# Kernel optimization log

Measured on AMD Instinct MI355X. Metric: run time of the kernel, lower is better.

## Reference

```python
import jax, jax.numpy as jnp
import numpy as np

L, D, H, B, N = 4, 1024, 16, 4, 1024
DK = D // H
BN_EPS = 1e-5


def conv1x1(x, W, b):
    # x: (B, C_in, N), W: (C_out, C_in), b: (C_out,)
    return jnp.einsum('oc,bcn->bon', W, x) + b[:, None]


def setup_inputs() -> dict:
    key = jax.random.key(0)
    ks = jax.random.split(key, 17)
    s = 0.02
    inp = {
        'motion_feats': jax.random.normal(ks[0], (B, D, N), dtype=jnp.float32),
        'Wq': jax.random.normal(ks[1], (L, D, D), dtype=jnp.float32) * s,
        'bq': jax.random.normal(ks[2], (L, D), dtype=jnp.float32) * s,
        'Wk': jax.random.normal(ks[3], (L, D, D), dtype=jnp.float32) * s,
        'bk': jax.random.normal(ks[4], (L, D), dtype=jnp.float32) * s,
        'Wv': jax.random.normal(ks[5], (L, D, D), dtype=jnp.float32) * s,
        'bv': jax.random.normal(ks[6], (L, D), dtype=jnp.float32) * s,
        'Wm': jax.random.normal(ks[7], (L, D, D), dtype=jnp.float32) * s,
        'bm': jax.random.normal(ks[8], (L, D), dtype=jnp.float32) * s,
        'Wp1': jax.random.normal(ks[9], (L, 2 * D, 2 * D), dtype=jnp.float32) * s,
        'bp1': jax.random.normal(ks[10], (L, 2 * D), dtype=jnp.float32) * s,
        'bn_gamma': 1.0 + 0.1 * jax.random.normal(ks[11], (L, 2 * D), dtype=jnp.float32),
        'bn_beta': 0.1 * jax.random.normal(ks[12], (L, 2 * D), dtype=jnp.float32),
        'bn_mean': 0.1 * jax.random.normal(ks[13], (L, 2 * D), dtype=jnp.float32),
        'bn_var': 0.5 + jax.random.uniform(ks[14], (L, 2 * D), dtype=jnp.float32),
        'Wp2': jax.random.normal(ks[15], (L, D, 2 * D), dtype=jnp.float32) * s,
        'bp2': jnp.zeros((L, D), dtype=jnp.float32),  # init.constant_(bias, 0)
    }
    return inp


def _mha_layer(x, Wq, bq, Wk, bk, Wv, bv, Wm, bm, Wp1, bp1, g, bta, mu, var, Wp2, bp2):
    # x: (B, D, N)
    q = conv1x1(x, Wq, bq).reshape(B, DK, H, N)
    k = conv1x1(x, Wk, bk).reshape(B, DK, H, N)
    v = conv1x1(x, Wv, bv).reshape(B, DK, H, N)
    scores = jnp.einsum('bdhn,bdhm->bhnm', q, k) / jnp.sqrt(jnp.float32(DK))
    w = jax.nn.softmax(scores, axis=-1)
    attn = jnp.einsum('bhnm,bdhm->bdhn', w, v).reshape(B, D, N)
    merged = conv1x1(attn, Wm, bm)
    h = jnp.concatenate([merged, x], axis=1)  # (B, 2D, N)
    h = conv1x1(h, Wp1, bp1)
    # BatchNorm1d in eval mode (running stats)
    h = g[:, None] * (h - mu[:, None]) * jax.lax.rsqrt(var[:, None] + BN_EPS) + bta[:, None]
    h = jax.nn.relu(h)
    return conv1x1(h, Wp2, bp2)


def reference(motion_feats, Wq, bq, Wk, bk, Wv, bv, Wm, bm, Wp1, bp1,
              bn_gamma, bn_beta, bn_mean, bn_var, Wp2, bp2):
    x = motion_feats
    for l in range(L):
        attn_out = _mha_layer(x, Wq[l], bq[l], Wk[l], bk[l], Wv[l], bv[l],
                              Wm[l], bm[l], Wp1[l], bp1[l],
                              bn_gamma[l], bn_beta[l], bn_mean[l], bn_var[l],
                              Wp2[l], bp2[l])
        x = x + attn_out
    return x
```

## Files before the change

### kernel.cpp

```cpp
#include <hip/hip_runtime.h>

typedef unsigned short u16;
typedef __attribute__((ext_vector_type(8))) short bf16x8;
typedef __attribute__((ext_vector_type(4))) float f32x4;

#define B_ 4
#define D_ 1024
#define N_ 1024
#define H_ 16
#define DK_ 64

__device__ inline float bf2f(u16 x) {
    union { unsigned u; float f; } c; c.u = ((unsigned)x) << 16; return c.f;
}
__device__ inline u16 f2bf(float f) {
    union { float f; unsigned u; } c; c.f = f;
    unsigned r = c.u + 0x7fff + ((c.u >> 16) & 1);
    return (u16)(r >> 16);
}

#if __has_builtin(__builtin_amdgcn_exp2f)
#define EXP2(x) __builtin_amdgcn_exp2f(x)
#else
#define EXP2(x) __expf((x) * 0.6931471805599453f)
#endif

__device__ inline bf16x8 load8(const void* p, size_t idx, int fl) {
    if (!fl) return *(const bf16x8*)((const u16*)p + idx);
    const float* fp = (const float*)p + idx;
    f32x4 a = *(const f32x4*)fp;
    f32x4 b = *(const f32x4*)(fp + 4);
    bf16x8 r;
    #pragma unroll
    for (int j = 0; j < 4; ++j) {
        ((u16*)&r)[j]     = f2bf(a[j]);
        ((u16*)&r)[4 + j] = f2bf(b[j]);
    }
    return r;
}

__global__ __launch_bounds__(256) void k_cvt(
    const float* __restrict__ src, u16* __restrict__ dst, int n8)
{
    int i = blockIdx.x * 256 + threadIdx.x;
    if (i < n8) {
        const f32x4* s = (const f32x4*)src;
        f32x4 a = s[2 * i], b = s[2 * i + 1];
        bf16x8 r;
        #pragma unroll
        for (int j = 0; j < 4; ++j) {
            ((u16*)&r)[j]     = f2bf(a[j]);
            ((u16*)&r)[4 + j] = f2bf(b[j]);
        }
        ((bf16x8*)dst)[i] = r;
    }
}

__device__ __forceinline__ void gload16(const u16* g, u16* l) {
    __builtin_amdgcn_global_load_lds(
        (const __attribute__((address_space(1))) void*)g,
        (__attribute__((address_space(3))) void*)l, 16, 0, 0);
}

template<int ROWS>
__device__ __forceinline__ void stage_rows(const u16* __restrict__ g, int ld,
                                           int k0, u16* L, int wave)
{
    #pragma unroll
    for (int i = 0; i < ROWS / 64; ++i)
        gload16(g + (size_t)(i * 64) * ld + k0, L + i * 2048 + wave * 512);
}

template<int MT, int NT>
__device__ inline void gemm_bf16(const u16* __restrict__ A, int lda,
                                 const u16* __restrict__ Bt, size_t eoff,
                                 int ldb, int K, int m0, int n0,
                                 u16* lds, f32x4 acc[MT/32][NT/32])
{
    constexpr int FM = MT / 32, FN = NT / 32;
    constexpr int TSZ = (MT + NT) * 32;
    const int tid  = threadIdx.x;
    const int wave = tid >> 6, lane = tid & 63;
    const int quad = lane >> 4, l15 = lane & 15;
    const int wm = (wave >> 1) * (MT / 2);
    const int wn = (wave & 1) * (NT / 2);

    const u16* ga = A + (size_t)(m0 + (tid >> 2)) * lda + ((tid & 3) << 3);
    const u16* gb = Bt + eoff + (size_t)(n0 + (tid >> 2)) * ldb + ((tid & 3) << 3);

    stage_rows<MT>(ga, lda, 0, lds, wave);
    stage_rows<NT>(gb, ldb, 0, lds + MT * 32, wave);
    __syncthreads();

    int buf = 0;
    for (int k0 = 0; k0 < K; k0 += 32) {
        const u16* La = lds + buf * TSZ;
        const u16* Lb = La + MT * 32;

        if (k0 + 32 < K) {
            u16* Na = lds + (buf ^ 1) * TSZ;
            stage_rows<MT>(ga, lda, k0 + 32, Na, wave);
            stage_rows<NT>(gb, ldb, k0 + 32, Na + MT * 32, wave);
        }

        bf16x8 af[FM], bv[FN];
        #pragma unroll
        for (int f = 0; f < FM; ++f)
            af[f] = *(const bf16x8*)&La[(wm + f * 16 + l15) * 32 + quad * 8];
        #pragma unroll
        for (int f = 0; f < FN; ++f)
            bv[f] = *(const bf16x8*)&Lb[(wn + f * 16 + l15) * 32 + quad * 8];
        #pragma unroll
        for (int fm = 0; fm < FM; ++fm)
            #pragma unroll
            for (int fn = 0; fn < FN; ++fn)
                acc[fm][fn] = __builtin_amdgcn_mfma_f32_16x16x32_bf16(
                    af[fm], bv[fn], acc[fm][fn], 0, 0, 0);

        __syncthreads();
        buf ^= 1;
    }
}

template<int MT, int NT>
__device__ inline void gemm_core(const u16* __restrict__ A, int lda,
                                 const void* __restrict__ Bt, size_t eoff,
                                 int ldb, int fl,
                                 int K, int m0, int n0,
                                 u16* lds, f32x4 acc[MT/32][NT/32])
{
    constexpr int FM = MT / 32, FN = NT / 32;
    constexpr int CA = MT * 4 / 256, CB = NT * 4 / 256;
    const int tid  = threadIdx.x;
    const int wave = tid >> 6, lane = tid & 63;
    const int quad = lane >> 4, l15 = lane & 15;
    const int wm = (wave >> 1) * (MT / 2);
    const int wn = (wave & 1) * (NT / 2);

    int arow[CA], acol[CA], brow[CB], bcol[CB];
    #pragma unroll
    for (int i = 0; i < CA; ++i) { int x = tid + i * 256; arow[i] = x >> 2; acol[i] = (x & 3) << 3; }
    #pragma unroll
    for (int i = 0; i < CB; ++i) { int x = tid + i * 256; brow[i] = x >> 2; bcol[i] = (x & 3) << 3; }

    bf16x8 pa[CA], pb[CB];
    #pragma unroll
    for (int i = 0; i < CA; ++i)
        pa[i] = *(const bf16x8*)(A + (size_t)(m0 + arow[i]) * lda + acol[i]);
    #pragma unroll
    for (int i = 0; i < CB; ++i)
        pb[i] = load8(Bt, eoff + (size_t)(n0 + brow[i]) * ldb + bcol[i], fl);

    int buf = 0;
    for (int k0 = 0; k0 < K; k0 += 32) {
        u16* La = lds + buf * ((MT + NT) * 40);
        u16* Lb = La + MT * 40;
        #pragma unroll
        for (int i = 0; i < CA; ++i) *(bf16x8*)&La[arow[i] * 40 + acol[i]] = pa[i];
        #pragma unroll
        for (int i = 0; i < CB; ++i) *(bf16x8*)&Lb[brow[i] * 40 + bcol[i]] = pb[i];
        __syncthreads();

        if (k0 + 32 < K) {
            #pragma unroll
            for (int i = 0; i < CA; ++i)
                pa[i] = *(const bf16x8*)(A + (size_t)(m0 + arow[i]) * lda + k0 + 32 + acol[i]);
            #pragma unroll
            for (int i = 0; i < CB; ++i)
                pb[i] = load8(Bt, eoff + (size_t)(n0 + brow[i]) * ldb + k0 + 32 + bcol[i], fl);
        }

        bf16x8 af[FM], bv[FN];
        #pragma unroll
        for (int f = 0; f < FM; ++f)
            af[f] = *(bf16x8*)&La[(wm + f * 16 + l15) * 40 + quad * 8];
        #pragma unroll
        for (int f = 0; f < FN; ++f)
            bv[f] = *(bf16x8*)&Lb[(wn + f * 16 + l15) * 40 + quad * 8];
        #pragma unroll
        for (int fm = 0; fm < FM; ++fm)
            #pragma unroll
            for (int fn = 0; fn < FN; ++fn)
                acc[fm][fn] = __builtin_amdgcn_mfma_f32_16x16x32_bf16(
                    af[fm], bv[fn], acc[fm][fn], 0, 0, 0);
        buf ^= 1;
    }
}

#define EPI_SETUP \
    const int tid = threadIdx.x; \
    const int wave = tid >> 6, lane = tid & 63; \
    const int quad = lane >> 4, l15 = lane & 15;

__global__ __launch_bounds__(256) void k_qkv(
    const u16* __restrict__ xb,
    const void* __restrict__ Wq, const void* __restrict__ Wk, const void* __restrict__ Wv,
    const float* __restrict__ bq, const float* __restrict__ bk, const float* __restrict__ bv,
    int fl, u16* __restrict__ qh, u16* __restrict__ kh, u16* __restrict__ vt)
{
    __shared__ u16 lds[2 * (128 + 128) * 40];
    int mat = blockIdx.z;
    const void* W     = mat == 0 ? Wq : (mat == 1 ? Wk : Wv);
    const float* bias = mat == 0 ? bq : (mat == 1 ? bk : bv);
    int m0 = blockIdx.x * 128, n0 = blockIdx.y * 128;

    f32x4 acc[4][4];
    #pragma unroll
    for (int i = 0; i < 4; ++i)
        #pragma unroll
        for (int j = 0; j < 4; ++j) acc[i][j] = f32x4{0.f, 0.f, 0.f, 0.f};

    if (fl) gemm_core<128, 128>(xb, D_, W, 0, D_, 1, D_, m0, n0, lds, acc);
    else    gemm_bf16<128, 128>(xb, D_, (const u16*)W, 0, D_, D_, m0, n0, lds, acc);

    EPI_SETUP
    const int wm = (wave >> 1) * 64, wn = (wave & 1) * 64;
    #pragma unroll
    for (int fm = 0; fm < 4; ++fm)
        #pragma unroll
        for (int fn = 0; fn < 4; ++fn) {
            int n = n0 + wn + fn * 16 + l15;
            float bz = bias[n];
            int h = n & 15, dk = n >> 4;
            #pragma unroll
            for (int r = 0; r < 4; ++r) {
                int m = m0 + wm + fm * 16 + quad * 4 + r;
                int b = m >> 10, pos = m & 1023;
                int bh = b * H_ + h;
                u16 o = f2bf(acc[fm][fn][r] + bz);
                if (mat == 0) {
                    qh[(((size_t)bh * N_ + pos) * DK_ + dk)] = o;
                } else if (mat == 1) {
                    size_t kidx = (((size_t)bh * 64 + (pos >> 4)) << 10)
                                + ((dk >> 5) << 9) + (((dk >> 3) & 3) << 7)
                                + ((pos & 15) << 3) + (dk & 7);
                    kh[kidx] = o;
                } else {
                    size_t vidx = (((size_t)bh * 32 + (pos >> 5)) << 11)
                                + ((dk >> 4) << 9) + (((pos >> 3) & 3) << 7)
                                + ((dk & 15) << 3) + (pos & 7);
                    vt[vidx] = o;
                }
            }
        }
}

__global__ __launch_bounds__(64) void k_flash(
    const u16* __restrict__ qh, const u16* __restrict__ kh,
    const u16* __restrict__ vt, u16* __restrict__ at)
{
    __shared__ u16 P[16 * 136];

    const int bh = blockIdx.y, b = bh >> 4, h = bh & 15;
    const int lane = threadIdx.x;
    const int quad = lane >> 4, l15 = lane & 15;
    const int q0 = blockIdx.x * 16;

    const u16* Q  = qh + (size_t)bh * N_ * DK_;
    const u16* Kf = kh + ((size_t)bh << 16);
    const u16* Vf = vt + ((size_t)bh << 16);

    bf16x8 qf[2];
    #pragma unroll
    for (int kk = 0; kk < 2; ++kk)
        qf[kk] = *(const bf16x8*)&Q[(size_t)(q0 + l15) * DK_ + kk * 32 + quad * 8];

    f32x4 acc_o[4];
    #pragma unroll
    for (int j = 0; j < 4; ++j) acc_o[j] = f32x4{0.f, 0.f, 0.f, 0.f};
    float mrow[4], lrow[4];
    #pragma unroll
    for (int r = 0; r < 4; ++r) { mrow[r] = -1e30f; lrow[r] = 0.f; }

    const float c = 0.18033688011112042f;

    #pragma unroll 2
    for (int mt = 0; mt < 8; ++mt) {
        f32x4 s[8];
        #pragma unroll
        for (int j = 0; j < 8; ++j) s[j] = f32x4{0.f, 0.f, 0.f, 0.f};
        #pragma unroll
        for (int kk = 0; kk < 2; ++kk) {
            bf16x8 kf[8];
            #pragma unroll
            for (int fn = 0; fn < 8; ++fn)
                kf[fn] = *(const bf16x8*)&Kf[((size_t)(mt * 8 + fn) << 10)
                                             + (kk << 9) + (quad << 7) + (l15 << 3)];
            #pragma unroll
            for (int fn = 0; fn < 8; ++fn)
                s[fn] = __builtin_amdgcn_mfma_f32_16x16x32_bf16(
                    qf[kk], kf[fn], s[fn], 0, 0, 0);
        }

        #pragma unroll
        for (int r = 0; r < 4; ++r) {
            float mx = s[0][r];
            #pragma unroll
            for (int fn = 1; fn < 8; ++fn) mx = fmaxf(mx, s[fn][r]);
            #pragma unroll
            for (int o = 1; o < 16; o <<= 1)
                mx = fmaxf(mx, __shfl_xor(mx, o, 64));
            float mn = fmaxf(mrow[r], mx);
            float al = EXP2((mrow[r] - mn) * c);
            float nmc = -mn * c;
            float rs = 0.f;
            #pragma unroll
            for (int fn = 0; fn < 8; ++fn) {
                float p = EXP2(fmaf(s[fn][r], c, nmc));
                s[fn][r] = p;
                rs += p;
            }
            #pragma unroll
            for (int o = 1; o < 16; o <<= 1)
                rs += __shfl_xor(rs, o, 64);
            lrow[r] = al * lrow[r] + rs;
            mrow[r] = mn;
            #pragma unroll
            for (int fn = 0; fn < 4; ++fn) acc_o[fn][r] *= al;
        }

        #pragma unroll
        for (int fn = 0; fn < 8; ++fn)
            #pragma unroll
            for (int r = 0; r < 4; ++r)
                P[(quad * 4 + r) * 136 + fn * 16 + l15] = f2bf(s[fn][r]);

        #pragma unroll
        for (int ks = 0; ks < 4; ++ks) {
            bf16x8 vf[4];
            #pragma unroll
            for (int fn = 0; fn < 4; ++fn)
                vf[fn] = *(const bf16x8*)&Vf[((size_t)(mt * 4 + ks) << 11)
                                             + (fn << 9) + (quad << 7) + (l15 << 3)];
            bf16x8 pf = *(bf16x8*)&P[l15 * 136 + ks * 32 + quad * 8];
            #pragma unroll
            for (int fn = 0; fn < 4; ++fn)
                acc_o[fn] = __builtin_amdgcn_mfma_f32_16x16x32_bf16(
                    pf, vf[fn], acc_o[fn], 0, 0, 0);
        }
    }

    #pragma unroll
    for (int r = 0; r < 4; ++r) {
        float inv = 1.f / lrow[r];
        int pos = q0 + quad * 4 + r;
        #pragma unroll
        for (int fn = 0; fn < 4; ++fn) {
            int dk = fn * 16 + l15;
            at[((size_t)(b * N_ + pos)) * D_ + dk * 16 + h] =
                f2bf(acc_o[fn][r] * inv);
        }
    }
}

__global__ __launch_bounds__(256) void k_merged(
    const u16* __restrict__ at, const void* __restrict__ Wm,
    const float* __restrict__ bm, int fl, u16* __restrict__ mg)
{
    __shared__ u16 lds[2 * (64 + 128) * 40];
    int m0 = blockIdx.x * 64, n0 = blockIdx.y * 128;

    f32x4 acc[2][4];
    #pragma unroll
    for (int i = 0; i < 2; ++i)
        #pragma unroll
        for (int j = 0; j < 4; ++j) acc[i][j] = f32x4{0.f, 0.f, 0.f, 0.f};

    if (fl) gemm_core<64, 128>(at, D_, Wm, 0, D_, 1, D_, m0, n0, lds, acc);
    else    gemm_bf16<64, 128>(at, D_, (const u16*)Wm, 0, D_, D_, m0, n0, lds, acc);

    EPI_SETUP
    const int wm = (wave >> 1) * 32, wn = (wave & 1) * 64;
    #pragma unroll
    for (int fm = 0; fm < 2; ++fm)
        #pragma unroll
        for (int fn = 0; fn < 4; ++fn) {
            int n = n0 + wn + fn * 16 + l15;
            float bz = bm[n];
            #pragma unroll
            for (int r = 0; r < 4; ++r) {
                int m = m0 + wm + fm * 16 + quad * 4 + r;
                mg[(size_t)m * D_ + n] = f2bf(acc[fm][fn][r] + bz);
            }
        }
}

__global__ __launch_bounds__(256) void k_p1(
    const u16* __restrict__ mg, const u16* __restrict__ xb,
    const void* __restrict__ Wp1, int fl,
    const float* __restrict__ bp1, const float* __restrict__ gam,
    const float* __restrict__ bet, const float* __restrict__ mu,
    const float* __restrict__ var, u16* __restrict__ h2)
{
    __shared__ u16 lds[2 * (128 + 128) * 40];
    int m0 = blockIdx.x * 128, n0 = blockIdx.y * 128;

    f32x4 acc[4][4];
    #pragma unroll
    for (int i = 0; i < 4; ++i)
        #pragma unroll
        for (int j = 0; j < 4; ++j) acc[i][j] = f32x4{0.f, 0.f, 0.f, 0.f};

    if (fl) {
        gemm_core<128, 128>(mg, D_, Wp1, 0,    2048, 1, D_, m0, n0, lds, acc);
        gemm_core<128, 128>(xb, D_, Wp1, 1024, 2048, 1, D_, m0, n0, lds, acc);
    } else {
        gemm_bf16<128, 128>(mg, D_, (const u16*)Wp1, 0,    2048, D_, m0, n0, lds, acc);
        gemm_bf16<128, 128>(xb, D_, (const u16*)Wp1, 1024, 2048, D_, m0, n0, lds, acc);
    }

    EPI_SETUP
    const int wm = (wave >> 1) * 64, wn = (wave & 1) * 64;
    #pragma unroll
    for (int fm = 0; fm < 4; ++fm)
        #pragma unroll
        for (int fn = 0; fn < 4; ++fn) {
            int n = n0 + wn + fn * 16 + l15;
            float bz = bp1[n];
            float sc = gam[n] * rsqrtf(var[n] + 1e-5f);
            float mn = mu[n], be = bet[n];
            #pragma unroll
            for (int r = 0; r < 4; ++r) {
                int m = m0 + wm + fm * 16 + quad * 4 + r;
                float y = (acc[fm][fn][r] + bz - mn) * sc + be;
                h2[(size_t)m * 2048 + n] = f2bf(fmaxf(y, 0.f));
            }
        }
}

__global__ __launch_bounds__(256) void k_p2(
    const u16* __restrict__ h2, const void* __restrict__ Wp2,
    const float* __restrict__ bp2, int fl,
    float* __restrict__ xf, u16* __restrict__ xb)
{
    __shared__ u16 lds[2 * (64 + 128) * 40];
    int m0 = blockIdx.x * 64, n0 = blockIdx.y * 128;

    f32x4 acc[2][4];
    #pragma unroll
    for (int i = 0; i < 2; ++i)
        #pragma unroll
        for (int j = 0; j < 4; ++j) acc[i][j] = f32x4{0.f, 0.f, 0.f, 0.f};

    if (fl) gemm_core<64, 128>(h2, 2048, Wp2, 0, 2048, 1, 2048, m0, n0, lds, acc);
    else    gemm_bf16<64, 128>(h2, 2048, (const u16*)Wp2, 0, 2048, 2048, m0, n0, lds, acc);

    EPI_SETUP
    const int wm = (wave >> 1) * 32, wn = (wave & 1) * 64;
    #pragma unroll
    for (int fm = 0; fm < 2; ++fm)
        #pragma unroll
        for (int fn = 0; fn < 4; ++fn) {
            int n = n0 + wn + fn * 16 + l15;
            float bz = bp2[n];
            #pragma unroll
            for (int r = 0; r < 4; ++r) {
                int m = m0 + wm + fm * 16 + quad * 4 + r;
                size_t ad = (size_t)m * D_ + n;
                float nv = xf[ad] + acc[fm][fn][r] + bz;
                xf[ad] = nv;
                xb[ad] = f2bf(nv);
            }
        }
}

__global__ __launch_bounds__(256) void k_tin(
    const float* __restrict__ mo, float* __restrict__ xf, u16* __restrict__ xb)
{
    __shared__ float t[32][33];
    int b = blockIdx.z;
    int p0 = blockIdx.x * 32, c0 = blockIdx.y * 32;
    int tx = threadIdx.x & 31, ty = threadIdx.x >> 5;
    const float* src = mo + ((size_t)b * D_ + c0) * N_ + p0;
    #pragma unroll
    for (int k = 0; k < 4; ++k)
        t[ty + k * 8][tx] = src[(size_t)(ty + k * 8) * N_ + tx];
    __syncthreads();
    size_t base = ((size_t)b * N_ + p0) * D_ + c0;
    #pragma unroll
    for (int k = 0; k < 4; ++k) {
        float v = t[tx][ty + k * 8];
        xf[base + (size_t)(ty + k * 8) * D_ + tx] = v;
        xb[base + (size_t)(ty + k * 8) * D_ + tx] = f2bf(v);
    }
}

__global__ __launch_bounds__(256) void k_tout(
    const float* __restrict__ xf, float* __restrict__ out)
{
    __shared__ float t[32][33];
    int b = blockIdx.z;
    int c0 = blockIdx.x * 32, p0 = blockIdx.y * 32;
    int tx = threadIdx.x & 31, ty = threadIdx.x >> 5;
    const float* src = xf + ((size_t)b * N_ + p0) * D_ + c0;
    #pragma unroll
    for (int k = 0; k < 4; ++k)
        t[ty + k * 8][tx] = src[(size_t)(ty + k * 8) * D_ + tx];
    __syncthreads();
    float* dst = out + ((size_t)b * D_ + c0) * N_ + p0;
    #pragma unroll
    for (int k = 0; k < 4; ++k)
        dst[(size_t)(ty + k * 8) * N_ + tx] = t[tx][ty + k * 8];
}

extern "C" void kernel_launch(void* const* d_in, const int* in_sizes, int n_in,
                              void* d_out, int out_size, void* d_ws, size_t ws_size,
                              hipStream_t stream)
{
    const float* mo  = (const float*)d_in[0];
    const float* Wqf = (const float*)d_in[1];
    const float* bq  = (const float*)d_in[2];
    const float* Wkf = (const float*)d_in[3];
    const float* bk  = (const float*)d_in[4];
    const float* Wvf = (const float*)d_in[5];
    const float* bv  = (const float*)d_in[6];
    const float* Wmf = (const float*)d_in[7];
    const float* bm  = (const float*)d_in[8];
    const float* Wp1f= (const float*)d_in[9];
    const float* bp1 = (const float*)d_in[10];
    const float* gam = (const float*)d_in[11];
    const float* bet = (const float*)d_in[12];
    const float* mu  = (const float*)d_in[13];
    const float* var = (const float*)d_in[14];
    const float* Wp2f= (const float*)d_in[15];
    const float* bp2 = (const float*)d_in[16];

    char* ws = (char*)d_ws;
    float* xf = (float*)ws;
    u16* xb   = (u16*)(ws + (16ull << 20));
    u16* qh   = (u16*)(ws + (24ull << 20));
    u16* kh   = (u16*)(ws + (32ull << 20));
    u16* vt   = (u16*)(ws + (40ull << 20));
    u16* at   = (u16*)(ws + (48ull << 20));
    u16* mg   = qh;
    u16* h2   = kh;
    u16* wb   = (u16*)(ws + (56ull << 20));

    const size_t S1 = 1048576;
    const size_t SP1 = 4194304;
    const size_t SP2 = 2097152;
    const size_t OQ = 0, OK4 = 4 * S1, OV = 8 * S1, OM = 12 * S1,
                 OP1 = 16 * S1, OP2 = OP1 + 4 * SP1;

    int mode;
    if (ws_size >= (137ull << 20)) mode = 2;
    else if (ws_size >= (77ull << 20)) mode = 1;
    else mode = 0;
    const int fl = (mode == 0) ? 1 : 0;

    dim3 blk(256);
    if (mode == 2) {
        k_cvt<<<2048, blk, 0, stream>>>(Wqf,  wb + OQ,  524288);
        k_cvt<<<2048, blk, 0, stream>>>(Wkf,  wb + OK4, 524288);
        k_cvt<<<2048, blk, 0, stream>>>(Wvf,  wb + OV,  524288);
        k_cvt<<<2048, blk, 0, stream>>>(Wmf,  wb + OM,  524288);
        k_cvt<<<8192, blk, 0, stream>>>(Wp1f, wb + OP1, 2097152);
        k_cvt<<<4096, blk, 0, stream>>>(Wp2f, wb + OP2, 1048576);
    }

    k_tin<<<dim3(32, 32, 4), blk, 0, stream>>>(mo, xf, xb);

    for (int l = 0; l < 4; ++l) {
        const void *pWq, *pWk, *pWv, *pWm, *pWp1, *pWp2;
        if (mode == 2) {
            pWq  = wb + OQ  + (size_t)l * S1;
            pWk  = wb + OK4 + (size_t)l * S1;
            pWv  = wb + OV  + (size_t)l * S1;
            pWm  = wb + OM  + (size_t)l * S1;
            pWp1 = wb + OP1 + (size_t)l * SP1;
            pWp2 = wb + OP2 + (size_t)l * SP2;
        } else if (mode == 1) {
            k_cvt<<<512,  blk, 0, stream>>>(Wqf  + l * S1,  wb,               131072);
            k_cvt<<<512,  blk, 0, stream>>>(Wkf  + l * S1,  wb + S1,          131072);
            k_cvt<<<512,  blk, 0, stream>>>(Wvf  + l * S1,  wb + 2 * S1,      131072);
            k_cvt<<<512,  blk, 0, stream>>>(Wmf  + l * S1,  wb + 3 * S1,      131072);
            k_cvt<<<2048, blk, 0, stream>>>(Wp1f + l * SP1, wb + 4 * S1,      524288);
            k_cvt<<<1024, blk, 0, stream>>>(Wp2f + l * SP2, wb + 4 * S1 + SP1, 262144);
            pWq = wb; pWk = wb + S1; pWv = wb + 2 * S1; pWm = wb + 3 * S1;
            pWp1 = wb + 4 * S1; pWp2 = wb + 4 * S1 + SP1;
        } else {
            pWq  = Wqf  + l * S1;
            pWk  = Wkf  + l * S1;
            pWv  = Wvf  + l * S1;
            pWm  = Wmf  + l * S1;
            pWp1 = Wp1f + l * SP1;
            pWp2 = Wp2f + l * SP2;
        }

        k_qkv<<<dim3(32, 8, 3), blk, 0, stream>>>(
            xb, pWq, pWk, pWv, bq + l * D_, bk + l * D_, bv + l * D_, fl, qh, kh, vt);
        k_flash<<<dim3(64, 64), dim3(64), 0, stream>>>(qh, kh, vt, at);
        k_merged<<<dim3(64, 8), blk, 0, stream>>>(at, pWm, bm + l * D_, fl, mg);
        k_p1<<<dim3(32, 16), blk, 0, stream>>>(
            mg, xb, pWp1, fl, bp1 + l * 2048, gam + l * 2048, bet + l * 2048,
            mu + l * 2048, var + l * 2048, h2);
        k_p2<<<dim3(64, 8), blk, 0, stream>>>(
            h2, pWp2, bp2 + l * D_, fl, xf, xb);
    }
    k_tout<<<dim3(32, 32, 4), blk, 0, stream>>>(xf, (float*)d_out);
}
```

Before: 1.194 ms.

## Triple-buffer LDS in bf16 GEMM with vmcnt waits instead of full barriers

Converts the double-buffered global-to-LDS pipeline in gemm_bf16 into a three-stage ring. Loads are issued two K-steps ahead, and each step waits with s_waitcnt vmcnt on only the older load group before a raw s_barrier. This replaces the two __syncthreads per iteration, so global loads can overlap more with MFMA work. LDS arrays are resized to three stages, which raises shared memory per block and could lower occupancy. Correctness relies on the global_load_lds counts matching the hardcoded vmcnt values, and the fl=1 path (gemm_core) uses the same arrays with its own layout.

```diff
diff --git a/kernel.cpp b/kernel.cpp
--- a/kernel.cpp
+++ b/kernel.cpp
@@ -71,6 +71,15 @@
         gload16(g + (size_t)(i * 64) * ld + k0, L + i * 2048 + wave * 512);
 }
 
+template<int N>
+__device__ __forceinline__ void waitcnt_vm() {
+    if constexpr (N == 0)      asm volatile("s_waitcnt vmcnt(0)" ::: "memory");
+    else if constexpr (N == 3) asm volatile("s_waitcnt vmcnt(3)" ::: "memory");
+    else if constexpr (N == 4) asm volatile("s_waitcnt vmcnt(4)" ::: "memory");
+    else if constexpr (N == 6) asm volatile("s_waitcnt vmcnt(6)" ::: "memory");
+    else if constexpr (N == 8) asm volatile("s_waitcnt vmcnt(8)" ::: "memory");
+}
+
 template<int MT, int NT>
 __device__ inline void gemm_bf16(const u16* __restrict__ A, int lda,
                                  const u16* __restrict__ Bt, size_t eoff,
@@ -79,6 +88,7 @@
 {
     constexpr int FM = MT / 32, FN = NT / 32;
     constexpr int TSZ = (MT + NT) * 32;
+    constexpr int NL  = MT / 64 + NT / 64;
     const int tid  = threadIdx.x;
     const int wave = tid >> 6, lane = tid & 63;
     const int quad = lane >> 4, l15 = lane & 15;
@@ -90,19 +100,18 @@
 
     stage_rows<MT>(ga, lda, 0, lds, wave);
     stage_rows<NT>(gb, ldb, 0, lds + MT * 32, wave);
-    __syncthreads();
-
-    int buf = 0;
-    for (int k0 = 0; k0 < K; k0 += 32) {
-        const u16* La = lds + buf * TSZ;
+    if (K > 32) {
+        stage_rows<MT>(ga, lda, 32, lds + TSZ, wave);
+        stage_rows<NT>(gb, ldb, 32, lds + TSZ + MT * 32, wave);
+    }
+
+    int b0 = 0;
+    for (int k0 = 0; k0 < K - 32; k0 += 32) {
+        waitcnt_vm<NL>();
+        __builtin_amdgcn_s_barrier();
+
+        const u16* La = lds + b0 * TSZ;
         const u16* Lb = La + MT * 32;
-
-        if (k0 + 32 < K) {
-            u16* Na = lds + (buf ^ 1) * TSZ;
-            stage_rows<MT>(ga, lda, k0 + 32, Na, wave);
-            stage_rows<NT>(gb, ldb, k0 + 32, Na + MT * 32, wave);
-        }
-
         bf16x8 af[FM], bv[FN];
         #pragma unroll
         for (int f = 0; f < FM; ++f)
@@ -110,6 +119,14 @@
         #pragma unroll
         for (int f = 0; f < FN; ++f)
             bv[f] = *(const bf16x8*)&Lb[(wn + f * 16 + l15) * 32 + quad * 8];
+
+        if (k0 + 64 < K) {
+            int b2 = b0 + 2; if (b2 >= 3) b2 -= 3;
+            u16* Nx = lds + b2 * TSZ;
+            stage_rows<MT>(ga, lda, k0 + 64, Nx, wave);
+            stage_rows<NT>(gb, ldb, k0 + 64, Nx + MT * 32, wave);
+        }
+
         #pragma unroll
         for (int fm = 0; fm < FM; ++fm)
             #pragma unroll
@@ -117,9 +134,29 @@
                 acc[fm][fn] = __builtin_amdgcn_mfma_f32_16x16x32_bf16(
                     af[fm], bv[fn], acc[fm][fn], 0, 0, 0);
 
-        __syncthreads();
-        buf ^= 1;
-    }
+        b0 = (b0 == 2) ? 0 : b0 + 1;
+    }
+
+    waitcnt_vm<0>();
+    __builtin_amdgcn_s_barrier();
+    {
+        const u16* La = lds + b0 * TSZ;
+        const u16* Lb = La + MT * 32;
+        bf16x8 af[FM], bv[FN];
+        #pragma unroll
+        for (int f = 0; f < FM; ++f)
+            af[f] = *(const bf16x8*)&La[(wm + f * 16 + l15) * 32 + quad * 8];
+        #pragma unroll
+        for (int f = 0; f < FN; ++f)
+            bv[f] = *(const bf16x8*)&Lb[(wn + f * 16 + l15) * 32 + quad * 8];
+        #pragma unroll
+        for (int fm = 0; fm < FM; ++fm)
+            #pragma unroll
+            for (int fn = 0; fn < FN; ++fn)
+                acc[fm][fn] = __builtin_amdgcn_mfma_f32_16x16x32_bf16(
+                    af[fm], bv[fn], acc[fm][fn], 0, 0, 0);
+    }
+    __syncthreads();
 }
 
 template<int MT, int NT>
@@ -198,7 +235,7 @@
     const float* __restrict__ bq, const float* __restrict__ bk, const float* __restrict__ bv,
     int fl, u16* __restrict__ qh, u16* __restrict__ kh, u16* __restrict__ vt)
 {
-    __shared__ u16 lds[2 * (128 + 128) * 40];
+    __shared__ u16 lds[3 * (128 + 128) * 32];
     int mat = blockIdx.z;
     const void* W     = mat == 0 ? Wq : (mat == 1 ? Wk : Wv);
     const float* bias = mat == 0 ? bq : (mat == 1 ? bk : bv);
@@ -357,7 +394,7 @@
     const u16* __restrict__ at, const void* __restrict__ Wm,
     const float* __restrict__ bm, int fl, u16* __restrict__ mg)
 {
-    __shared__ u16 lds[2 * (64 + 128) * 40];
+    __shared__ u16 lds[3 * (64 + 128) * 32];
     int m0 = blockIdx.x * 64, n0 = blockIdx.y * 128;
 
     f32x4 acc[2][4];
@@ -392,7 +429,7 @@
     const float* __restrict__ bet, const float* __restrict__ mu,
     const float* __restrict__ var, u16* __restrict__ h2)
 {
-    __shared__ u16 lds[2 * (128 + 128) * 40];
+    __shared__ u16 lds[3 * (128 + 128) * 32];
     int m0 = blockIdx.x * 128, n0 = blockIdx.y * 128;
 
     f32x4 acc[4][4];
@@ -433,7 +470,7 @@
     const float* __restrict__ bp2, int fl,
     float* __restrict__ xf, u16* __restrict__ xb)
 {
-    __shared__ u16 lds[2 * (64 + 128) * 40];
+    __shared__ u16 lds[3 * (64 + 128) * 32];
     int m0 = blockIdx.x * 64, n0 = blockIdx.y * 128;
 
     f32x4 acc[2][4];
```

New measurement: 1.188 ms. Within noise of the previous version (-0.5%).
